# Kernel optimization log

Hardware: AMD Instinct MI355X
Metric: run time of the kernel (lower is better)

The kernel has to match this reference:

```python
import jax, jax.numpy as jnp
import numpy as np
from jax import lax

EPS = 1e-5
DN = ('NCDHW', 'OIDHW', 'NCDHW')
CHANNELS = [4, 32, 64, 128, 256, 512]
OUT_CH = 256


def _conv_s2(x, w):
    # 3x3x3 conv, stride 2, padding 1 (torchsparse spnn.Conv3d on densified grid)
    return lax.conv_general_dilated(x, w, window_strides=(2, 2, 2),
                                    padding=[(1, 1)] * 3, dimension_numbers=DN)


def _bn_relu(x, g, b, m, v):
    # inference BatchNorm (running stats) + ReLU, fused elementwise
    inv = g * lax.rsqrt(v + EPS)           # [C]
    shp = (1, -1, 1, 1, 1)
    return jnp.maximum(x * inv.reshape(shp) + (b - m * inv).reshape(shp), 0.0)


def setup_inputs() -> dict:
    key = jax.random.key(0)
    ks = jax.random.split(key, 32)
    inp = {}
    inp['x'] = jax.random.normal(ks[0], (2, 4, 128, 128, 128), dtype=jnp.float32)
    ki = 1
    for i in range(5):
        cin, cout = CHANNELS[i], CHANNELS[i + 1]
        fan_in = cin * 27
        inp[f'w{i+1}'] = jax.random.normal(ks[ki], (cout, cin, 3, 3, 3), dtype=jnp.float32) / np.sqrt(fan_in); ki += 1
        inp[f'g{i+1}'] = 1.0 + 0.1 * jax.random.normal(ks[ki], (cout,), dtype=jnp.float32); ki += 1
        inp[f'b{i+1}'] = 0.1 * jax.random.normal(ks[ki], (cout,), dtype=jnp.float32); ki += 1
        inp[f'm{i+1}'] = 0.1 * jax.random.normal(ks[ki], (cout,), dtype=jnp.float32); ki += 1
        inp[f'v{i+1}'] = jax.random.uniform(ks[ki], (cout,), dtype=jnp.float32, minval=0.5, maxval=1.5); ki += 1
    inp['w_out'] = jax.random.normal(ks[ki], (OUT_CH, 512, 1, 1, 1), dtype=jnp.float32) / np.sqrt(512.0)
    return inp


def reference(x, w1, g1, b1, m1, v1, w2, g2, b2, m2, v2, w3, g3, b3, m3, v3,
              w4, g4, b4, m4, v4, w5, g5, b5, m5, v5, w_out):
    h = _bn_relu(_conv_s2(x, w1), g1, b1, m1, v1)   # [B,32,64,64,64]
    h = _bn_relu(_conv_s2(h, w2), g2, b2, m2, v2)   # [B,64,32,32,32]
    h = _bn_relu(_conv_s2(h, w3), g3, b3, m3, v3)   # [B,128,16,16,16]
    h = _bn_relu(_conv_s2(h, w4), g4, b4, m4, v4)   # [B,256,8,8,8]
    h = _bn_relu(_conv_s2(h, w5), g5, b5, m5, v5)   # [B,512,4,4,4]
    # 1x1x1 output conv, stride 1
    out = lax.conv_general_dilated(h, w_out, window_strides=(1, 1, 1),
                                   padding=[(0, 0)] * 3, dimension_numbers=DN)
    return out  # [B,256,4,4,4]
```

## Files before the change

### kernel.cpp

```cpp
#include <hip/hip_runtime.h>

static constexpr float kEps = 1e-5f;

using bf16x8 = __attribute__((ext_vector_type(8))) short;
using f32x4 = __attribute__((ext_vector_type(4))) float;
typedef unsigned short ushort_t;

constexpr int ilog2(int n) { return n <= 1 ? 0 : 1 + ilog2(n / 2); }

__device__ inline unsigned bf_rne(float v) {
  unsigned u = __float_as_uint(v);
  return (u + 0x7FFFu + ((u >> 16) & 1u)) >> 16;
}
__device__ inline void split_bf(float v, unsigned short& h, unsigned short& l) {
  unsigned hb = bf_rne(v);
  h = (unsigned short)hb;
  float hf = __uint_as_float(hb << 16);
  l = (unsigned short)bf_rne(v - hf);
}

template <int CIN, int COUT>
__global__ __launch_bounds__(256) void repack_kernel(
    const float* __restrict__ w, const float* __restrict__ g,
    const float* __restrict__ b, const float* __restrict__ m,
    const float* __restrict__ v, float* __restrict__ wT,
    float* __restrict__ bias) {
  int idx = blockIdx.x * 256 + threadIdx.x;
  constexpr int total = COUT * CIN * 27;
  if (idx < COUT) {
    float inv = g[idx] * rsqrtf(v[idx] + kEps);
    bias[idx] = b[idx] - m[idx] * inv;
  }
  if (idx < total) {
    int cout = idx % COUT;
    int ck = idx / COUT;
    int cin = ck / 27;
    int k = ck % 27;
    float inv = g[cout] * rsqrtf(v[cout] + kEps);
    wT[idx] = w[(cout * CIN + cin) * 27 + k] * inv;
  }
}

template <int CIN, int COUT>
__global__ __launch_bounds__(256) void repack_bf16(
    const float* __restrict__ w, const float* __restrict__ g,
    const float* __restrict__ b, const float* __restrict__ m,
    const float* __restrict__ v, unsigned short* __restrict__ wh,
    unsigned short* __restrict__ wl, float* __restrict__ bias) {
  int idx = blockIdx.x * 256 + threadIdx.x;
  constexpr int total = 27 * COUT * CIN;
  constexpr int LC = ilog2(CIN), LO = ilog2(COUT);
  if (idx < COUT) {
    float inv = g[idx] * rsqrtf(v[idx] + kEps);
    bias[idx] = b[idx] - m[idx] * inv;
  }
  if (idx < total) {
    int ci = idx & (CIN - 1);
    int t = idx >> LC;
    int co = t & (COUT - 1);
    int tap = t >> LO;
    float inv = g[co] * rsqrtf(v[co] + kEps);
    float val = w[((size_t)co * CIN + ci) * 27 + tap] * inv;
    unsigned short h, l;
    split_bf(val, h, l);
    wh[idx] = h;
    wl[idx] = l;
  }
}

__global__ __launch_bounds__(256) void repack_wout(const float* __restrict__ w,
                                                   float* __restrict__ wt) {
  int idx = blockIdx.x * 256 + threadIdx.x;
  int co = idx & 255;
  int c = idx >> 8;
  wt[idx] = w[(size_t)co * 512 + c];
}

__global__ __launch_bounds__(256) void conv1_direct(
    const float* __restrict__ in, const float* __restrict__ wT,
    const float* __restrict__ bias, unsigned short* __restrict__ outh,
    unsigned short* __restrict__ outl) {
  constexpr int DI = 128, CIN = 4, COUT = 32;
  int tid = blockIdx.x * 256 + threadIdx.x;
  int x = tid & 63;
  int t = tid >> 6;
  int y = t & 63;
  t >>= 6;
  int z = t & 63;
  int bb = t >> 6;

  float acc[COUT];
#pragma unroll
  for (int i = 0; i < COUT; ++i) acc[i] = 0.f;

  const float* inb = in + (size_t)bb * CIN * DI * DI * DI;
  for (int cin = 0; cin < CIN; ++cin) {
    const float* inc = inb + (size_t)cin * DI * DI * DI;
#pragma unroll
    for (int kz = 0; kz < 3; ++kz) {
      int iz = 2 * z + kz - 1;
      if (iz < 0) continue;
#pragma unroll
      for (int ky = 0; ky < 3; ++ky) {
        int iy = 2 * y + ky - 1;
        if (iy < 0) continue;
        const float* row = inc + ((size_t)iz * DI + iy) * DI;
#pragma unroll
        for (int kx = 0; kx < 3; ++kx) {
          int ix = 2 * x + kx - 1;
          float xv = (ix >= 0) ? row[ix] : 0.f;
          const float* wp = wT + ((size_t)cin * 27 + (kz * 3 + ky) * 3 + kx) * COUT;
#pragma unroll
          for (int i = 0; i < COUT; ++i) acc[i] = fmaf(xv, wp[i], acc[i]);
        }
      }
    }
  }
  int pidx = (z & 1) * 4 + (y & 1) * 2 + (x & 1);
  size_t sub = (((size_t)(z >> 1) * 32) + (y >> 1)) * 32 + (x >> 1);
  size_t op = (((size_t)bb * 8 + pidx) * 32768 + sub) * COUT;
#pragma unroll
  for (int i = 0; i < COUT; ++i) {
    float r = fmaxf(acc[i] + bias[i], 0.f);
    unsigned short h, l;
    split_bf(r, h, l);
    outh[op + i] = h;
    outl[op + i] = l;
  }
}

template <int CIN, int COUT, int DO, int SK, int MREP>
__global__ __launch_bounds__(256) void conv_mfma(
    const unsigned short* __restrict__ inh, const unsigned short* __restrict__ inl,
    const unsigned short* __restrict__ wh, const unsigned short* __restrict__ wl,
    const float* __restrict__ bias, unsigned short* __restrict__ outh,
    unsigned short* __restrict__ outl, float* __restrict__ partial) {
  constexpr int M = 2 * DO * DO * DO;
  constexpr int TAPS = 27 / SK;
  constexpr int KCPT = CIN / 32;
  constexpr int LD = ilog2(DO);
  constexpr int SUB = DO * DO * DO;

  const int lane = threadIdx.x & 63;
  const int wv = threadIdx.x >> 6;
  const int mWave = (blockIdx.x * 4 + wv) * (MREP * 16);
  const int nBase = blockIdx.y * 64;
  const int skid = blockIdx.z;
  const int mlane = lane & 15;
  const int kgrp = lane >> 4;

  int xf[MREP], yf[MREP], zf[MREP], bf_[MREP];
#pragma unroll
  for (int f = 0; f < MREP; ++f) {
    int m = mWave + f * 16 + mlane;
    xf[f] = m & (DO - 1);
    yf[f] = (m >> LD) & (DO - 1);
    zf[f] = (m >> (2 * LD)) & (DO - 1);
    bf_[f] = m >> (3 * LD);
  }

  f32x4 acc[MREP][4];
#pragma unroll
  for (int f = 0; f < MREP; ++f)
#pragma unroll
    for (int q = 0; q < 4; ++q) acc[f][q] = (f32x4){0.f, 0.f, 0.f, 0.f};

  for (int tp = 0; tp < TAPS; ++tp) {
    const int tap = skid * TAPS + tp;
    const int kz = tap / 9;
    const int kr = tap - kz * 9;
    const int ky = kr / 3;
    const int kx = kr - ky * 3;
    const int pidx = (kz != 1) * 4 + (ky != 1) * 2 + (kx != 1);
    const int dz = (kz == 0), dy = (ky == 0), dx = (kx == 0);

    const size_t woff = (size_t)tap * COUT * CIN + (size_t)(nBase + mlane) * CIN + kgrp * 8;
    const unsigned short* wbh = wh + woff;
    const unsigned short* wbl = wl + woff;

    long long aoff[MREP];
    bool valid[MREP];
#pragma unroll
    for (int f = 0; f < MREP; ++f) {
      int sx = xf[f] - dx, sy = yf[f] - dy, sz = zf[f] - dz;
      valid[f] = ((sx | sy | sz) >= 0);
      aoff[f] = ((long long)(bf_[f] * 8 + pidx) * SUB + (sz * DO + sy) * DO + sx) * CIN +
                kgrp * 8;
    }

#pragma unroll
    for (int kc = 0; kc < KCPT; ++kc) {
      bf16x8 Ah[MREP], Al[MREP];
#pragma unroll
      for (int f = 0; f < MREP; ++f) {
        Ah[f] = (bf16x8){0, 0, 0, 0, 0, 0, 0, 0};
        Al[f] = (bf16x8){0, 0, 0, 0, 0, 0, 0, 0};
        if (valid[f]) {
          Ah[f] = *reinterpret_cast<const bf16x8*>(inh + aoff[f] + kc * 32);
          Al[f] = *reinterpret_cast<const bf16x8*>(inl + aoff[f] + kc * 32);
        }
      }
#pragma unroll
      for (int nq = 0; nq < 4; ++nq) {
        bf16x8 Bh = *reinterpret_cast<const bf16x8*>(wbh + (size_t)nq * 16 * CIN + kc * 32);
        bf16x8 Bl = *reinterpret_cast<const bf16x8*>(wbl + (size_t)nq * 16 * CIN + kc * 32);
#pragma unroll
        for (int f = 0; f < MREP; ++f) {
          acc[f][nq] = __builtin_amdgcn_mfma_f32_16x16x32_bf16(Ah[f], Bh, acc[f][nq], 0, 0, 0);
          acc[f][nq] = __builtin_amdgcn_mfma_f32_16x16x32_bf16(Ah[f], Bl, acc[f][nq], 0, 0, 0);
          acc[f][nq] = __builtin_amdgcn_mfma_f32_16x16x32_bf16(Al[f], Bh, acc[f][nq], 0, 0, 0);
        }
      }
    }
  }

  if constexpr (SK == 1) {
    constexpr int HD = DO / 2;
#pragma unroll
    for (int f = 0; f < MREP; ++f) {
#pragma unroll
      for (int nq = 0; nq < 4; ++nq) {
        const int n = nBase + nq * 16 + mlane;
        const float bv = bias[n];
#pragma unroll
        for (int r = 0; r < 4; ++r) {
          const int mrow = mWave + f * 16 + kgrp * 4 + r;
          const int ox = mrow & (DO - 1);
          const int oy = (mrow >> LD) & (DO - 1);
          const int oz = (mrow >> (2 * LD)) & (DO - 1);
          const int ob = mrow >> (3 * LD);
          const int pp = (oz & 1) * 4 + (oy & 1) * 2 + (ox & 1);
          const size_t sub = (((size_t)(oz >> 1) * HD) + (oy >> 1)) * HD + (ox >> 1);
          const size_t addr = (((size_t)ob * 8 + pp) * (HD * HD * HD) + sub) * COUT + n;
          float vv = fmaxf(acc[f][nq][r] + bv, 0.f);
          unsigned short h, l;
          split_bf(vv, h, l);
          outh[addr] = h;
          outl[addr] = l;
        }
      }
    }
  } else {
#pragma unroll
    for (int f = 0; f < MREP; ++f) {
#pragma unroll
      for (int nq = 0; nq < 4; ++nq) {
        const int n = nBase + nq * 16 + mlane;
#pragma unroll
        for (int r = 0; r < 4; ++r) {
          const int mrow = mWave + f * 16 + kgrp * 4 + r;
          partial[((size_t)skid * M + mrow) * COUT + n] = acc[f][nq][r];
        }
      }
    }
  }
}

template <int COUT, int SK, int M, int DOP, bool F32OUT>
__global__ __launch_bounds__(256) void reduce_split(
    const float* __restrict__ partial, const float* __restrict__ bias,
    unsigned short* __restrict__ oh, unsigned short* __restrict__ ol,
    float* __restrict__ of) {
  constexpr int LD = ilog2(DOP);
  constexpr int HD = DOP / 2;
  int idx = blockIdx.x * 256 + threadIdx.x;
  int n = idx & (COUT - 1);
  int mrow = idx / COUT;
  float s = 0.f;
#pragma unroll
  for (int k = 0; k < SK; ++k) s += partial[(size_t)k * M * COUT + idx];
  float v = fmaxf(s + bias[n], 0.f);
  if constexpr (F32OUT) {
    of[idx] = v;
  } else {
    const int ox = mrow & (DOP - 1);
    const int oy = (mrow >> LD) & (DOP - 1);
    const int oz = (mrow >> (2 * LD)) & (DOP - 1);
    const int ob = mrow >> (3 * LD);
    const int pp = (oz & 1) * 4 + (oy & 1) * 2 + (ox & 1);
    const size_t sub = (((size_t)(oz >> 1) * HD) + (oy >> 1)) * HD + (ox >> 1);
    const size_t addr = (((size_t)ob * 8 + pp) * (HD * HD * HD) + sub) * COUT + n;
    unsigned short h, l;
    split_bf(v, h, l);
    oh[addr] = h;
    ol[addr] = l;
  }
}

__global__ __launch_bounds__(256) void conv1x1_final(
    const float* __restrict__ h5, const float* __restrict__ wt,
    float* __restrict__ out) {
  int p = blockIdx.x;
  int co = threadIdx.x;
  int b = p >> 6;
  int s = p & 63;
  const float* hp = h5 + (size_t)p * 512;
  float acc = 0.f;
#pragma unroll 8
  for (int c = 0; c < 512; ++c) acc = fmaf(hp[c], wt[(size_t)c * 256 + co], acc);
  out[((size_t)b * 256 + co) * 64 + s] = acc;
}

extern "C" void kernel_launch(void* const* d_in, const int* in_sizes, int n_in,
                              void* d_out, int out_size, void* d_ws,
                              size_t ws_size, hipStream_t stream) {
  const float* x = (const float*)d_in[0];
  const float* w1 = (const float*)d_in[1];
  const float* g1 = (const float*)d_in[2];
  const float* bb1 = (const float*)d_in[3];
  const float* m1 = (const float*)d_in[4];
  const float* v1 = (const float*)d_in[5];
  const float* w2 = (const float*)d_in[6];
  const float* g2 = (const float*)d_in[7];
  const float* bb2 = (const float*)d_in[8];
  const float* m2 = (const float*)d_in[9];
  const float* v2 = (const float*)d_in[10];
  const float* w3 = (const float*)d_in[11];
  const float* g3 = (const float*)d_in[12];
  const float* bb3 = (const float*)d_in[13];
  const float* m3 = (const float*)d_in[14];
  const float* v3 = (const float*)d_in[15];
  const float* w4 = (const float*)d_in[16];
  const float* g4 = (const float*)d_in[17];
  const float* bb4 = (const float*)d_in[18];
  const float* m4 = (const float*)d_in[19];
  const float* v4 = (const float*)d_in[20];
  const float* w5 = (const float*)d_in[21];
  const float* g5 = (const float*)d_in[22];
  const float* bb5 = (const float*)d_in[23];
  const float* m5 = (const float*)d_in[24];
  const float* v5 = (const float*)d_in[25];
  const float* w_out = (const float*)d_in[26];
  (void)in_sizes; (void)n_in; (void)out_size; (void)ws_size;

  char* base = (char*)d_ws;
  size_t off = 0;
  auto take = [&](size_t bytes) {
    char* p = base + off;
    off = (off + bytes + 255) & ~(size_t)255;
    return p;
  };
  float* wt1 = (float*)take(3456 * 4);
  unsigned short* w2h = (unsigned short*)take(55296 * 2);
  unsigned short* w2l = (unsigned short*)take(55296 * 2);
  unsigned short* w3h = (unsigned short*)take(221184 * 2);
  unsigned short* w3l = (unsigned short*)take(221184 * 2);
  unsigned short* w4h = (unsigned short*)take(884736 * 2);
  unsigned short* w4l = (unsigned short*)take(884736 * 2);
  unsigned short* w5h = (unsigned short*)take(3538944 * 2);
  unsigned short* w5l = (unsigned short*)take(3538944 * 2);
  float* woutT = (float*)take(131072 * 4);
  float* bs1 = (float*)take(32 * 4);
  float* bs2 = (float*)take(64 * 4);
  float* bs3 = (float*)take(128 * 4);
  float* bs4 = (float*)take(256 * 4);
  float* bs5 = (float*)take(512 * 4);
  unsigned short* h1h = (unsigned short*)take((size_t)16777216 * 2);
  unsigned short* h1l = (unsigned short*)take((size_t)16777216 * 2);
  unsigned short* h2h = (unsigned short*)take((size_t)4194304 * 2);
  unsigned short* h2l = (unsigned short*)take((size_t)4194304 * 2);

  char* AR = (char*)h1h;
  float* p3 = (float*)AR;
  float* p4 = (float*)AR;
  float* p5 = (float*)AR;
  char* AR2 = AR + ((size_t)16 << 20);
  unsigned short* h3h = (unsigned short*)AR2;
  unsigned short* h3l = (unsigned short*)(AR2 + 2097152);
  unsigned short* h4h = (unsigned short*)(AR2 + 2 * 2097152);
  unsigned short* h4l = (unsigned short*)(AR2 + 2 * 2097152 + 524288);
  float* h5 = (float*)(AR2 + 2 * 2097152 + 2 * 524288);

  repack_kernel<4, 32><<<(3456 + 255) / 256, 256, 0, stream>>>(
      w1, g1, bb1, m1, v1, wt1, bs1);
  repack_bf16<32, 64><<<(55296 + 255) / 256, 256, 0, stream>>>(
      w2, g2, bb2, m2, v2, w2h, w2l, bs2);
  repack_bf16<64, 128><<<(221184 + 255) / 256, 256, 0, stream>>>(
      w3, g3, bb3, m3, v3, w3h, w3l, bs3);
  repack_bf16<128, 256><<<(884736 + 255) / 256, 256, 0, stream>>>(
      w4, g4, bb4, m4, v4, w4h, w4l, bs4);
  repack_bf16<256, 512><<<(3538944 + 255) / 256, 256, 0, stream>>>(
      w5, g5, bb5, m5, v5, w5h, w5l, bs5);
  repack_wout<<<512, 256, 0, stream>>>(w_out, woutT);

  conv1_direct<<<2048, 256, 0, stream>>>(x, wt1, bs1, h1h, h1l);

  conv_mfma<32, 64, 32, 1, 2><<<dim3(512, 1, 1), 256, 0, stream>>>(
      h1h, h1l, w2h, w2l, bs2, h2h, h2l, nullptr);

  conv_mfma<64, 128, 16, 3, 2><<<dim3(64, 2, 3), 256, 0, stream>>>(
      h2h, h2l, w3h, w3l, bs3, nullptr, nullptr, p3);
  reduce_split<128, 3, 8192, 16, false><<<4096, 256, 0, stream>>>(
      p3, bs3, h3h, h3l, nullptr);

  conv_mfma<128, 256, 8, 9, 1><<<dim3(16, 4, 9), 256, 0, stream>>>(
      h3h, h3l, w4h, w4l, bs4, nullptr, nullptr, p4);
  reduce_split<256, 9, 1024, 8, false><<<1024, 256, 0, stream>>>(
      p4, bs4, h4h, h4l, nullptr);

  conv_mfma<256, 512, 4, 27, 1><<<dim3(2, 8, 27), 256, 0, stream>>>(
      h4h, h4l, w5h, w5l, bs5, nullptr, nullptr, p5);
  reduce_split<512, 27, 128, 4, true><<<256, 256, 0, stream>>>(
      p5, bs5, nullptr, nullptr, h5);

  conv1x1_final<<<128, 256, 0, stream>>>(h5, woutT, (float*)d_out);
}
```

Baseline: 421.6 us.

## Merge repack kernels, pack conv1 FMAs, fuse final reduce into 1x1 conv

Replaces six separate weight-repack launches with a single kernel that dispatches work by block range. Rewrites the first direct conv to use packed v_pk_fma_f32 on paired output channels and a vectorized two-float input load. Fuses the last split-K reduction with the 1x1 output conv through shared memory, removing one launch and the h5 round trip. The gains are mostly launch overhead plus a denser conv1 inner loop; the inline asm with asm volatile may limit compiler scheduling.

```diff
diff --git a/kernel.cpp b/kernel.cpp
--- a/kernel.cpp
+++ b/kernel.cpp
@@ -4,7 +4,7 @@
 
 using bf16x8 = __attribute__((ext_vector_type(8))) short;
 using f32x4 = __attribute__((ext_vector_type(4))) float;
-typedef unsigned short ushort_t;
+using f32x2 = __attribute__((ext_vector_type(2))) float;
 
 constexpr int ilog2(int n) { return n <= 1 ? 0 : 1 + ilog2(n / 2); }
 
@@ -19,14 +19,18 @@
   l = (unsigned short)bf_rne(v - hf);
 }
 
-template <int CIN, int COUT>
-__global__ __launch_bounds__(256) void repack_kernel(
-    const float* __restrict__ w, const float* __restrict__ g,
-    const float* __restrict__ b, const float* __restrict__ m,
-    const float* __restrict__ v, float* __restrict__ wT,
-    float* __restrict__ bias) {
-  int idx = blockIdx.x * 256 + threadIdx.x;
-  constexpr int total = COUT * CIN * 27;
+__device__ inline void pk_fma(f32x2& d, f32x2 a, f32x2 b) {
+  asm volatile("v_pk_fma_f32 %0, %1, %2, %0" : "+v"(d) : "v"(a), "v"(b));
+}
+
+__device__ inline void repack_s1_body(int idx, const float* __restrict__ w,
+                                      const float* __restrict__ g,
+                                      const float* __restrict__ b,
+                                      const float* __restrict__ m,
+                                      const float* __restrict__ v,
+                                      float* __restrict__ wT,
+                                      float* __restrict__ bias) {
+  constexpr int CIN = 4, COUT = 32, total = COUT * CIN * 27;
   if (idx < COUT) {
     float inv = g[idx] * rsqrtf(v[idx] + kEps);
     bias[idx] = b[idx] - m[idx] * inv;
@@ -42,12 +46,14 @@
 }
 
 template <int CIN, int COUT>
-__global__ __launch_bounds__(256) void repack_bf16(
-    const float* __restrict__ w, const float* __restrict__ g,
-    const float* __restrict__ b, const float* __restrict__ m,
-    const float* __restrict__ v, unsigned short* __restrict__ wh,
-    unsigned short* __restrict__ wl, float* __restrict__ bias) {
-  int idx = blockIdx.x * 256 + threadIdx.x;
+__device__ inline void repack_bf_body(int idx, const float* __restrict__ w,
+                                      const float* __restrict__ g,
+                                      const float* __restrict__ b,
+                                      const float* __restrict__ m,
+                                      const float* __restrict__ v,
+                                      unsigned short* __restrict__ wh,
+                                      unsigned short* __restrict__ wl,
+                                      float* __restrict__ bias) {
   constexpr int total = 27 * COUT * CIN;
   constexpr int LC = ilog2(CIN), LO = ilog2(COUT);
   if (idx < COUT) {
@@ -68,12 +74,34 @@
   }
 }
 
-__global__ __launch_bounds__(256) void repack_wout(const float* __restrict__ w,
-                                                   float* __restrict__ wt) {
-  int idx = blockIdx.x * 256 + threadIdx.x;
-  int co = idx & 255;
-  int c = idx >> 8;
-  wt[idx] = w[(size_t)co * 512 + c];
+__global__ __launch_bounds__(256) void repack_all(
+    const float* w1, const float* g1, const float* b1, const float* m1, const float* v1,
+    const float* w2, const float* g2, const float* b2, const float* m2, const float* v2,
+    const float* w3, const float* g3, const float* b3, const float* m3, const float* v3,
+    const float* w4, const float* g4, const float* b4, const float* m4, const float* v4,
+    const float* w5, const float* g5, const float* b5, const float* m5, const float* v5,
+    const float* w_out, float* wt1, unsigned short* w2h, unsigned short* w2l,
+    unsigned short* w3h, unsigned short* w3l, unsigned short* w4h, unsigned short* w4l,
+    unsigned short* w5h, unsigned short* w5l, float* woutT, float* bs1, float* bs2,
+    float* bs3, float* bs4, float* bs5) {
+  int blk = blockIdx.x;
+  int tid = threadIdx.x;
+  if (blk < 14) {
+    repack_s1_body(blk * 256 + tid, w1, g1, b1, m1, v1, wt1, bs1);
+  } else if (blk < 230) {
+    repack_bf_body<32, 64>((blk - 14) * 256 + tid, w2, g2, b2, m2, v2, w2h, w2l, bs2);
+  } else if (blk < 1094) {
+    repack_bf_body<64, 128>((blk - 230) * 256 + tid, w3, g3, b3, m3, v3, w3h, w3l, bs3);
+  } else if (blk < 4550) {
+    repack_bf_body<128, 256>((blk - 1094) * 256 + tid, w4, g4, b4, m4, v4, w4h, w4l, bs4);
+  } else if (blk < 18374) {
+    repack_bf_body<256, 512>((blk - 4550) * 256 + tid, w5, g5, b5, m5, v5, w5h, w5l, bs5);
+  } else {
+    int idx = (blk - 18374) * 256 + tid;
+    int co = idx & 255;
+    int c = idx >> 8;
+    woutT[idx] = w_out[(size_t)co * 512 + c];
+  }
 }
 
 __global__ __launch_bounds__(256) void conv1_direct(
@@ -89,9 +117,9 @@
   int z = t & 63;
   int bb = t >> 6;
 
-  float acc[COUT];
-#pragma unroll
-  for (int i = 0; i < COUT; ++i) acc[i] = 0.f;
+  f32x2 acc[16];
+#pragma unroll
+  for (int i = 0; i < 16; ++i) acc[i] = (f32x2){0.f, 0.f};
 
   const float* inb = in + (size_t)bb * CIN * DI * DI * DI;
   for (int cin = 0; cin < CIN; ++cin) {
@@ -105,13 +133,26 @@
         int iy = 2 * y + ky - 1;
         if (iy < 0) continue;
         const float* row = inc + ((size_t)iz * DI + iy) * DI;
-#pragma unroll
-        for (int kx = 0; kx < 3; ++kx) {
-          int ix = 2 * x + kx - 1;
-          float xv = (ix >= 0) ? row[ix] : 0.f;
-          const float* wp = wT + ((size_t)cin * 27 + (kz * 3 + ky) * 3 + kx) * COUT;
-#pragma unroll
-          for (int i = 0; i < COUT; ++i) acc[i] = fmaf(xv, wp[i], acc[i]);
+        f32x2 rv = *reinterpret_cast<const f32x2*>(row + 2 * x);
+        float xm = (x > 0) ? row[2 * x - 1] : 0.f;
+        const float* wbase = wT + ((size_t)cin * 27 + (kz * 3 + ky) * 3) * COUT;
+        {
+          f32x2 xv2 = (f32x2){xm, xm};
+#pragma unroll
+          for (int i = 0; i < 16; ++i)
+            pk_fma(acc[i], *reinterpret_cast<const f32x2*>(wbase + 2 * i), xv2);
+        }
+        {
+          f32x2 xv2 = (f32x2){rv.x, rv.x};
+#pragma unroll
+          for (int i = 0; i < 16; ++i)
+            pk_fma(acc[i], *reinterpret_cast<const f32x2*>(wbase + COUT + 2 * i), xv2);
+        }
+        {
+          f32x2 xv2 = (f32x2){rv.y, rv.y};
+#pragma unroll
+          for (int i = 0; i < 16; ++i)
+            pk_fma(acc[i], *reinterpret_cast<const f32x2*>(wbase + 2 * COUT + 2 * i), xv2);
         }
       }
     }
@@ -121,7 +162,7 @@
   size_t op = (((size_t)bb * 8 + pidx) * 32768 + sub) * COUT;
 #pragma unroll
   for (int i = 0; i < COUT; ++i) {
-    float r = fmaxf(acc[i] + bias[i], 0.f);
+    float r = fmaxf(acc[i >> 1][i & 1] + bias[i], 0.f);
     unsigned short h, l;
     split_bf(r, h, l);
     outh[op + i] = h;
@@ -256,11 +297,10 @@
   }
 }
 
-template <int COUT, int SK, int M, int DOP, bool F32OUT>
+template <int COUT, int SK, int M, int DOP>
 __global__ __launch_bounds__(256) void reduce_split(
     const float* __restrict__ partial, const float* __restrict__ bias,
-    unsigned short* __restrict__ oh, unsigned short* __restrict__ ol,
-    float* __restrict__ of) {
+    unsigned short* __restrict__ oh, unsigned short* __restrict__ ol) {
   constexpr int LD = ilog2(DOP);
   constexpr int HD = DOP / 2;
   int idx = blockIdx.x * 256 + threadIdx.x;
@@ -270,35 +310,39 @@
 #pragma unroll
   for (int k = 0; k < SK; ++k) s += partial[(size_t)k * M * COUT + idx];
   float v = fmaxf(s + bias[n], 0.f);
-  if constexpr (F32OUT) {
-    of[idx] = v;
-  } else {
-    const int ox = mrow & (DOP - 1);
-    const int oy = (mrow >> LD) & (DOP - 1);
-    const int oz = (mrow >> (2 * LD)) & (DOP - 1);
-    const int ob = mrow >> (3 * LD);
-    const int pp = (oz & 1) * 4 + (oy & 1) * 2 + (ox & 1);
-    const size_t sub = (((size_t)(oz >> 1) * HD) + (oy >> 1)) * HD + (ox >> 1);
-    const size_t addr = (((size_t)ob * 8 + pp) * (HD * HD * HD) + sub) * COUT + n;
-    unsigned short h, l;
-    split_bf(v, h, l);
-    oh[addr] = h;
-    ol[addr] = l;
-  }
-}
-
-__global__ __launch_bounds__(256) void conv1x1_final(
-    const float* __restrict__ h5, const float* __restrict__ wt,
-    float* __restrict__ out) {
+  const int ox = mrow & (DOP - 1);
+  const int oy = (mrow >> LD) & (DOP - 1);
+  const int oz = (mrow >> (2 * LD)) & (DOP - 1);
+  const int ob = mrow >> (3 * LD);
+  const int pp = (oz & 1) * 4 + (oy & 1) * 2 + (ox & 1);
+  const size_t sub = (((size_t)(oz >> 1) * HD) + (oy >> 1)) * HD + (ox >> 1);
+  const size_t addr = (((size_t)ob * 8 + pp) * (HD * HD * HD) + sub) * COUT + n;
+  unsigned short h, l;
+  split_bf(v, h, l);
+  oh[addr] = h;
+  ol[addr] = l;
+}
+
+__global__ __launch_bounds__(256) void final_fused(
+    const float* __restrict__ p5, const float* __restrict__ bias,
+    const float* __restrict__ wt, float* __restrict__ out) {
+  __shared__ float h[512];
   int p = blockIdx.x;
-  int co = threadIdx.x;
-  int b = p >> 6;
-  int s = p & 63;
-  const float* hp = h5 + (size_t)p * 512;
+  int t = threadIdx.x;
+#pragma unroll
+  for (int cc = 0; cc < 2; ++cc) {
+    int c = t + cc * 256;
+    float s = 0.f;
+#pragma unroll
+    for (int k = 0; k < 27; ++k) s += p5[((size_t)k * 128 + p) * 512 + c];
+    h[c] = fmaxf(s + bias[c], 0.f);
+  }
+  __syncthreads();
+  int b = p >> 6, sp = p & 63;
   float acc = 0.f;
 #pragma unroll 8
-  for (int c = 0; c < 512; ++c) acc = fmaf(hp[c], wt[(size_t)c * 256 + co], acc);
-  out[((size_t)b * 256 + co) * 64 + s] = acc;
+  for (int c = 0; c < 512; ++c) acc = fmaf(h[c], wt[(size_t)c * 256 + t], acc);
+  out[((size_t)b * 256 + t) * 64 + sp] = acc;
 }
 
 extern "C" void kernel_launch(void* const* d_in, const int* in_sizes, int n_in,
@@ -369,19 +413,12 @@
   unsigned short* h3l = (unsigned short*)(AR2 + 2097152);
   unsigned short* h4h = (unsigned short*)(AR2 + 2 * 2097152);
   unsigned short* h4l = (unsigned short*)(AR2 + 2 * 2097152 + 524288);
-  float* h5 = (float*)(AR2 + 2 * 2097152 + 2 * 524288);
-
-  repack_kernel<4, 32><<<(3456 + 255) / 256, 256, 0, stream>>>(
-      w1, g1, bb1, m1, v1, wt1, bs1);
-  repack_bf16<32, 64><<<(55296 + 255) / 256, 256, 0, stream>>>(
-      w2, g2, bb2, m2, v2, w2h, w2l, bs2);
-  repack_bf16<64, 128><<<(221184 + 255) / 256, 256, 0, stream>>>(
-      w3, g3, bb3, m3, v3, w3h, w3l, bs3);
-  repack_bf16<128, 256><<<(884736 + 255) / 256, 256, 0, stream>>>(
-      w4, g4, bb4, m4, v4, w4h, w4l, bs4);
-  repack_bf16<256, 512><<<(3538944 + 255) / 256, 256, 0, stream>>>(
-      w5, g5, bb5, m5, v5, w5h, w5l, bs5);
-  repack_wout<<<512, 256, 0, stream>>>(w_out, woutT);
+
+  repack_all<<<18886, 256, 0, stream>>>(
+      w1, g1, bb1, m1, v1, w2, g2, bb2, m2, v2, w3, g3, bb3, m3, v3,
+      w4, g4, bb4, m4, v4, w5, g5, bb5, m5, v5, w_out,
+      wt1, w2h, w2l, w3h, w3l, w4h, w4l, w5h, w5l, woutT,
+      bs1, bs2, bs3, bs4, bs5);
 
   conv1_direct<<<2048, 256, 0, stream>>>(x, wt1, bs1, h1h, h1l);
 
@@ -390,18 +427,14 @@
 
   conv_mfma<64, 128, 16, 3, 2><<<dim3(64, 2, 3), 256, 0, stream>>>(
       h2h, h2l, w3h, w3l, bs3, nullptr, nullptr, p3);
-  reduce_split<128, 3, 8192, 16, false><<<4096, 256, 0, stream>>>(
-      p3, bs3, h3h, h3l, nullptr);
+  reduce_split<128, 3, 8192, 16><<<4096, 256, 0, stream>>>(p3, bs3, h3h, h3l);
 
   conv_mfma<128, 256, 8, 9, 1><<<dim3(16, 4, 9), 256, 0, stream>>>(
       h3h, h3l, w4h, w4l, bs4, nullptr, nullptr, p4);
-  reduce_split<256, 9, 1024, 8, false><<<1024, 256, 0, stream>>>(
-      p4, bs4, h4h, h4l, nullptr);
+  reduce_split<256, 9, 1024, 8><<<1024, 256, 0, stream>>>(p4, bs4, h4h, h4l);
 
   conv_mfma<256, 512, 4, 27, 1><<<dim3(2, 8, 27), 256, 0, stream>>>(
       h4h, h4l, w5h, w5l, bs5, nullptr, nullptr, p5);
-  reduce_split<512, 27, 128, 4, true><<<256, 256, 0, stream>>>(
-      p5, bs5, nullptr, nullptr, h5);
-
-  conv1x1_final<<<128, 256, 0, stream>>>(h5, woutT, (float*)d_out);
-}
+
+  final_fused<<<128, 256, 0, stream>>>(p5, bs5, woutT, (float*)d_out);
+}
```

Measured after the change: 467.0 us. 1.11x slower.
